# Kernel tuning notes

Measured on AMD Instinct MI355X. Metric: run time of the kernel, lower is better.

## Reference

```python
import jax, jax.numpy as jnp
import numpy as np

EPS = 1.1920928955078125e-07  # torch.finfo(float32).eps, F.rms_norm default


def rms_norm(x):
    # F.rms_norm with no learnable weight: x / sqrt(mean(x^2) + eps)
    ms = jnp.mean(jnp.square(x), axis=-1, keepdims=True)
    return x * jax.lax.rsqrt(ms + EPS)


def setup_inputs() -> dict:
    key = jax.random.key(0)
    k1, k2, k3 = jax.random.split(key, 3)
    B, L, H, S = 4, 8192, 1024, 64
    x = jax.random.normal(k1, (B, L, H), dtype=jnp.float32)
    Ws = jax.random.normal(k2, (S, H), dtype=jnp.float32) * (1.0 / np.sqrt(H))
    Wo = jax.random.normal(k3, (H, S), dtype=jnp.float32) * (1.0 / np.sqrt(S))
    return {"x": x, "Ws": Ws, "Wo": Wo}


def reference(x, Ws, Wo):
    # state_proj: (B,L,H) @ (H,S) -> (B,L,S)
    state = jnp.einsum('blh,sh->bls', x, Ws)
    # running prefix-sum over sequence dim
    state = jnp.cumsum(state, axis=1)
    # RMSNorm over last dim, then out_proj back to hidden
    return jnp.einsum('bls,hs->blh', rms_norm(state), Wo)
```

## Files before the change

### kernel.cpp

```cpp
#include <hip/hip_runtime.h>
#include <hip/hip_bf16.h>


#define BB 4
#define LL 8192
#define HH 1024
#define SS 64
#define TL 64
#define CPB (LL / TL)
#define NCHUNK (BB * CPB)
#define EPS 1.1920928955078125e-07f

typedef __attribute__((ext_vector_type(8))) short bf16x8;
typedef __attribute__((ext_vector_type(4))) float f32x4;

__device__ __forceinline__ short bf16h(float v) {
    __hip_bfloat16 b = __float2bfloat16(v);
    return __builtin_bit_cast(short, b);
}
__device__ __forceinline__ float bf16tof(short s) {
    __hip_bfloat16 b = __builtin_bit_cast(__hip_bfloat16, s);
    return __bfloat162float(b);
}

__device__ __forceinline__ void stage_load(const float* __restrict__ src, int rstride,
                                           int tid, float4* v) {
    #pragma unroll
    for (int it = 0; it < 2; ++it) {
        const int row = it * 32 + (tid >> 3);
        const int k = (tid & 7) * 8;
        const float* p = src + (long)row * rstride + k;
        v[it * 2 + 0] = *(const float4*)p;
        v[it * 2 + 1] = *(const float4*)(p + 4);
    }
}
__device__ __forceinline__ void stage_write3(const float4* v, short (*th)[72],
                                             short (*tm)[72], short (*tl)[72], int tid) {
    #pragma unroll
    for (int it = 0; it < 2; ++it) {
        const int row = it * 32 + (tid >> 3);
        const int k = (tid & 7) * 8;
        const float f[8] = {v[it*2].x, v[it*2].y, v[it*2].z, v[it*2].w,
                            v[it*2+1].x, v[it*2+1].y, v[it*2+1].z, v[it*2+1].w};
        bf16x8 h8, m8, l8;
        #pragma unroll
        for (int j = 0; j < 8; ++j) {
            const short hb = bf16h(f[j]);
            const float r1 = f[j] - bf16tof(hb);
            const short mb = bf16h(r1);
            const float r2 = r1 - bf16tof(mb);
            h8[j] = hb; m8[j] = mb; l8[j] = bf16h(r2);
        }
        *(bf16x8*)&th[row][k] = h8;
        *(bf16x8*)&tm[row][k] = m8;
        *(bf16x8*)&tl[row][k] = l8;
    }
}

#define MFMA6(ACC, AH, AM, AL, BH, BM, BL)                                        \
    ACC = __builtin_amdgcn_mfma_f32_16x16x32_bf16(AH, BH, ACC, 0, 0, 0);          \
    ACC = __builtin_amdgcn_mfma_f32_16x16x32_bf16(AH, BM, ACC, 0, 0, 0);          \
    ACC = __builtin_amdgcn_mfma_f32_16x16x32_bf16(AM, BH, ACC, 0, 0, 0);          \
    ACC = __builtin_amdgcn_mfma_f32_16x16x32_bf16(AH, BL, ACC, 0, 0, 0);          \
    ACC = __builtin_amdgcn_mfma_f32_16x16x32_bf16(AL, BH, ACC, 0, 0, 0);          \
    ACC = __builtin_amdgcn_mfma_f32_16x16x32_bf16(AM, BM, ACC, 0, 0, 0);

__global__ __launch_bounds__(256) void k_proj(const float* __restrict__ x,
                                              const float* __restrict__ Ws,
                                              float* __restrict__ state,
                                              float* __restrict__ csum)
{
    __shared__ __align__(16) short Ah[64][72], Am[64][72], Al[64][72];
    __shared__ __align__(16) short Bh[64][72], Bm[64][72], Bl[64][72];
    float (*red)[65] = (float(*)[65])Ah;

    const int tid = threadIdx.x;
    const int lane = tid & 63, w = tid >> 6;
    const int l16 = lane & 15, lg = lane >> 4;
    const int wr = w >> 1, wc = w & 1;
    const int c = blockIdx.x;
    const float* xp = x + (long)c * TL * HH;

    f32x4 acc[2][2] = {};
    float4 va[4], vb[4];
    stage_load(xp, HH, tid, va);
    stage_load(Ws, HH, tid, vb);

    for (int kt = 0; kt < HH; kt += 64) {
        stage_write3(va, Ah, Am, Al, tid);
        stage_write3(vb, Bh, Bm, Bl, tid);
        __syncthreads();
        if (kt + 64 < HH) {
            stage_load(xp + kt + 64, HH, tid, va);
            stage_load(Ws + kt + 64, HH, tid, vb);
        }
        #pragma unroll
        for (int ks = 0; ks < 2; ++ks) {
            bf16x8 ah[2], am[2], al[2], bh[2], bm[2], bl[2];
            #pragma unroll
            for (int f = 0; f < 2; ++f) {
                const int ar = wr*32 + f*16 + l16, br = wc*32 + f*16 + l16;
                const int ko = ks*32 + lg*8;
                ah[f] = *(const bf16x8*)&Ah[ar][ko];
                am[f] = *(const bf16x8*)&Am[ar][ko];
                al[f] = *(const bf16x8*)&Al[ar][ko];
                bh[f] = *(const bf16x8*)&Bh[br][ko];
                bm[f] = *(const bf16x8*)&Bm[br][ko];
                bl[f] = *(const bf16x8*)&Bl[br][ko];
            }
            #pragma unroll
            for (int fi = 0; fi < 2; ++fi)
                #pragma unroll
                for (int fj = 0; fj < 2; ++fj) {
                    MFMA6(acc[fi][fj], ah[fi], am[fi], al[fi], bh[fj], bm[fj], bl[fj])
                }
        }
        __syncthreads();
    }

    float* sp = state + (long)c * (TL * SS);
    #pragma unroll
    for (int fi = 0; fi < 2; ++fi)
        #pragma unroll
        for (int fj = 0; fj < 2; ++fj) {
            float part = 0.f;
            #pragma unroll
            for (int r = 0; r < 4; ++r) {
                const int l = wr*32 + fi*16 + lg*4 + r;
                const int s = wc*32 + fj*16 + l16;
                sp[l * SS + s] = acc[fi][fj][r];
                part += acc[fi][fj][r];
            }
            red[(wr*2 + fi)*4 + lg][wc*32 + fj*16 + l16] = part;
        }
    __syncthreads();
    if (tid < 64) {
        float t = 0.f;
        #pragma unroll
        for (int g = 0; g < 16; ++g) t += red[g][tid];
        csum[(long)c * SS + tid] = t;
    }
}

__global__ __launch_bounds__(256) void k_scan(const float* __restrict__ csum,
                                              float* __restrict__ off)
{
    const int tid = threadIdx.x;
    const int lane = tid & 63;
    const int wid = (blockIdx.x * 256 + tid) >> 6;
    const int b = wid >> 6, s = wid & 63;
    const long base = (long)b * CPB * SS + s;

    float i0 = csum[base + (long)lane * SS];
    float i1 = csum[base + (long)(lane + 64) * SS];
    #pragma unroll
    for (int d = 1; d < 64; d <<= 1) {
        float n = __shfl_up(i0, d, 64); if (lane >= d) i0 += n;
    }
    #pragma unroll
    for (int d = 1; d < 64; d <<= 1) {
        float n = __shfl_up(i1, d, 64); if (lane >= d) i1 += n;
    }
    float tot0 = __shfl(i0, 63, 64);
    float e0 = __shfl_up(i0, 1, 64); if (lane == 0) e0 = 0.f;
    float e1 = __shfl_up(i1, 1, 64); if (lane == 0) e1 = 0.f;
    e1 += tot0;
    off[base + (long)lane * SS] = e0;
    off[base + (long)(lane + 64) * SS] = e1;
}

__global__ __launch_bounds__(256) void k_out(const float* __restrict__ state,
                                             const float* __restrict__ off,
                                             const float* __restrict__ Wo,
                                             float* __restrict__ out)
{
    __shared__ __align__(16) short Ah[64][72], Am[64][72], Al[64][72];
    __shared__ __align__(16) char pool[64 * 72 * 2 * 3];
    __shared__ float ssq[4][64];
    __shared__ float scale[64];
    float (*st)[65] = (float(*)[65])pool;
    short (*Bh)[72] = (short(*)[72])pool;
    short (*Bm)[72] = (short(*)[72])(pool + 64 * 72 * 2);
    short (*Bl)[72] = (short(*)[72])(pool + 64 * 72 * 4);

    const int tid = threadIdx.x;
    const int lane = tid & 63, w = tid >> 6;
    const int l16 = lane & 15, lg = lane >> 4;
    const int wr = w >> 1, wc = w & 1;
    const int c = blockIdx.x;

    float4 vw[4];
    stage_load(Wo, SS, tid, vw);

    const float* sp = state + (long)c * (TL * SS);
    #pragma unroll
    for (int i = 0; i < 4; ++i) {
        const int e = (i * 256 + tid) * 4;
        const int l = e >> 6, s = e & 63;
        const float4 v = *(const float4*)(sp + e);
        st[l][s] = v.x; st[l][s+1] = v.y; st[l][s+2] = v.z; st[l][s+3] = v.w;
    }
    __syncthreads();

    float sq = 0.f;
    for (int i = 0; i < 16; ++i) {
        const int s = w * 16 + i;
        float v = st[lane][s];
        #pragma unroll
        for (int d = 1; d < 64; d <<= 1) {
            const float n = __shfl_up(v, d, 64);
            if (lane >= d) v += n;
        }
        v += off[(long)c * SS + s];
        st[lane][s] = v;
        sq = fmaf(v, v, sq);
    }
    ssq[w][lane] = sq;
    __syncthreads();
    if (tid < 64) {
        const float t = ssq[0][tid] + ssq[1][tid] + ssq[2][tid] + ssq[3][tid];
        scale[tid] = rsqrtf(t * (1.f / 64.f) + EPS);
    }
    __syncthreads();

    {
        const int l = tid >> 2, s0 = (tid & 3) * 16;
        const float sc = scale[l];
        #pragma unroll
        for (int blk = 0; blk < 2; ++blk) {
            bf16x8 h8, m8, l8;
            #pragma unroll
            for (int j = 0; j < 8; ++j) {
                const float v = st[l][s0 + blk*8 + j] * sc;
                const short hb = bf16h(v);
                const float r1 = v - bf16tof(hb);
                const short mb = bf16h(r1);
                const float r2 = r1 - bf16tof(mb);
                h8[j] = hb; m8[j] = mb; l8[j] = bf16h(r2);
            }
            *(bf16x8*)&Ah[l][s0 + blk*8] = h8;
            *(bf16x8*)&Am[l][s0 + blk*8] = m8;
            *(bf16x8*)&Al[l][s0 + blk*8] = l8;
        }
    }
    __syncthreads();

    bf16x8 ah[2][2], am[2][2], al[2][2];
    #pragma unroll
    for (int f = 0; f < 2; ++f)
        #pragma unroll
        for (int ks = 0; ks < 2; ++ks) {
            const int ar = wr*32 + f*16 + l16, ko = ks*32 + lg*8;
            ah[f][ks] = *(const bf16x8*)&Ah[ar][ko];
            am[f][ks] = *(const bf16x8*)&Am[ar][ko];
            al[f][ks] = *(const bf16x8*)&Al[ar][ko];
        }

    const int b = c / CPB;
    const int l0 = (c % CPB) * TL;
    float* op = out + ((long)b * LL + l0) * HH;

    for (int ht = 0; ht < HH; ht += 64) {
        stage_write3(vw, Bh, Bm, Bl, tid);
        __syncthreads();
        if (ht + 64 < HH)
            stage_load(Wo + (long)(ht + 64) * SS, SS, tid, vw);
        f32x4 acc[2][2] = {};
        #pragma unroll
        for (int ks = 0; ks < 2; ++ks) {
            bf16x8 bh[2], bm[2], bl[2];
            #pragma unroll
            for (int f = 0; f < 2; ++f) {
                const int br = wc*32 + f*16 + l16, ko = ks*32 + lg*8;
                bh[f] = *(const bf16x8*)&Bh[br][ko];
                bm[f] = *(const bf16x8*)&Bm[br][ko];
                bl[f] = *(const bf16x8*)&Bl[br][ko];
            }
            #pragma unroll
            for (int fi = 0; fi < 2; ++fi)
                #pragma unroll
                for (int fj = 0; fj < 2; ++fj) {
                    MFMA6(acc[fi][fj], ah[fi][ks], am[fi][ks], al[fi][ks],
                          bh[fj], bm[fj], bl[fj])
                }
        }
        #pragma unroll
        for (int fi = 0; fi < 2; ++fi)
            #pragma unroll
            for (int fj = 0; fj < 2; ++fj)
                #pragma unroll
                for (int r = 0; r < 4; ++r) {
                    const int l = wr*32 + fi*16 + lg*4 + r;
                    const int h = wc*32 + fj*16 + l16;
                    op[(long)l * HH + ht + h] = acc[fi][fj][r];
                }
        __syncthreads();
    }
}

extern "C" void kernel_launch(void* const* d_in, const int* in_sizes, int n_in,
                              void* d_out, int out_size, void* d_ws, size_t ws_size,
                              hipStream_t stream) {
    const float* x  = (const float*)d_in[0];
    const float* Ws = (const float*)d_in[1];
    const float* Wo = (const float*)d_in[2];
    float* out = (float*)d_out;

    float* state = (float*)d_ws;
    float* csum  = state + (size_t)NCHUNK * SS * TL;
    float* off   = csum + (size_t)NCHUNK * SS;

    k_proj<<<NCHUNK, 256, 0, stream>>>(x, Ws, state, csum);
    k_scan<<<64, 256, 0, stream>>>(csum, off);
    k_out<<<NCHUNK, 256, 0, stream>>>(state, off, Wo, out);
}
```

Measured before the change: 279.8 us.

## Pre-split weights into bf16x3 once and use 512-thread blocks

Adds a prep kernel that splits Ws and Wo into high, mid and low bf16 parts once, so the projection and output kernels load pre-split weights instead of re-splitting them in every block. Both GEMM kernels move from 4 to 8 waves per block, each wave computing a 32x16 tile rather than 32x32. This is meant to cut redundant conversion ALU work and raise latency hiding. In exchange it adds a kernel launch, extra workspace traffic for three weight copies, and more LDS reads per MFMA from the smaller per-wave tiles.

```diff
diff --git a/kernel.cpp b/kernel.cpp
--- a/kernel.cpp
+++ b/kernel.cpp
@@ -23,37 +23,14 @@
     return __bfloat162float(b);
 }
 
-__device__ __forceinline__ void stage_load(const float* __restrict__ src, int rstride,
-                                           int tid, float4* v) {
-    #pragma unroll
-    for (int it = 0; it < 2; ++it) {
-        const int row = it * 32 + (tid >> 3);
-        const int k = (tid & 7) * 8;
-        const float* p = src + (long)row * rstride + k;
-        v[it * 2 + 0] = *(const float4*)p;
-        v[it * 2 + 1] = *(const float4*)(p + 4);
-    }
-}
-__device__ __forceinline__ void stage_write3(const float4* v, short (*th)[72],
-                                             short (*tm)[72], short (*tl)[72], int tid) {
-    #pragma unroll
-    for (int it = 0; it < 2; ++it) {
-        const int row = it * 32 + (tid >> 3);
-        const int k = (tid & 7) * 8;
-        const float f[8] = {v[it*2].x, v[it*2].y, v[it*2].z, v[it*2].w,
-                            v[it*2+1].x, v[it*2+1].y, v[it*2+1].z, v[it*2+1].w};
-        bf16x8 h8, m8, l8;
-        #pragma unroll
-        for (int j = 0; j < 8; ++j) {
-            const short hb = bf16h(f[j]);
-            const float r1 = f[j] - bf16tof(hb);
-            const short mb = bf16h(r1);
-            const float r2 = r1 - bf16tof(mb);
-            h8[j] = hb; m8[j] = mb; l8[j] = bf16h(r2);
-        }
-        *(bf16x8*)&th[row][k] = h8;
-        *(bf16x8*)&tm[row][k] = m8;
-        *(bf16x8*)&tl[row][k] = l8;
+__device__ __forceinline__ void split3_8(const float* f, bf16x8& h8, bf16x8& m8, bf16x8& l8) {
+    #pragma unroll
+    for (int j = 0; j < 8; ++j) {
+        const short hb = bf16h(f[j]);
+        const float r1 = f[j] - bf16tof(hb);
+        const short mb = bf16h(r1);
+        const float r2 = r1 - bf16tof(mb);
+        h8[j] = hb; m8[j] = mb; l8[j] = bf16h(r2);
     }
 }
 
@@ -65,10 +42,33 @@
     ACC = __builtin_amdgcn_mfma_f32_16x16x32_bf16(AL, BH, ACC, 0, 0, 0);          \
     ACC = __builtin_amdgcn_mfma_f32_16x16x32_bf16(AM, BM, ACC, 0, 0, 0);
 
-__global__ __launch_bounds__(256) void k_proj(const float* __restrict__ x,
-                                              const float* __restrict__ Ws,
-                                              float* __restrict__ state,
-                                              float* __restrict__ csum)
+__global__ __launch_bounds__(512) void k_prep(const float* __restrict__ Ws,
+                                              const float* __restrict__ Wo,
+                                              short* __restrict__ wsh, short* __restrict__ wsm,
+                                              short* __restrict__ wsl, short* __restrict__ woh,
+                                              short* __restrict__ wom, short* __restrict__ wol)
+{
+    const int i = blockIdx.x * 512 + threadIdx.x;
+    {
+        const float v = Ws[i];
+        const short h = bf16h(v); const float r1 = v - bf16tof(h);
+        const short m = bf16h(r1); const float r2 = r1 - bf16tof(m);
+        wsh[i] = h; wsm[i] = m; wsl[i] = bf16h(r2);
+    }
+    {
+        const float v = Wo[i];
+        const short h = bf16h(v); const float r1 = v - bf16tof(h);
+        const short m = bf16h(r1); const float r2 = r1 - bf16tof(m);
+        woh[i] = h; wom[i] = m; wol[i] = bf16h(r2);
+    }
+}
+
+__global__ __launch_bounds__(512, 4) void k_proj(const float* __restrict__ x,
+                                                 const short* __restrict__ wsh,
+                                                 const short* __restrict__ wsm,
+                                                 const short* __restrict__ wsl,
+                                                 float* __restrict__ state,
+                                                 float* __restrict__ csum)
 {
     __shared__ __align__(16) short Ah[64][72], Am[64][72], Al[64][72];
     __shared__ __align__(16) short Bh[64][72], Bm[64][72], Bl[64][72];
@@ -77,62 +77,76 @@
     const int tid = threadIdx.x;
     const int lane = tid & 63, w = tid >> 6;
     const int l16 = lane & 15, lg = lane >> 4;
-    const int wr = w >> 1, wc = w & 1;
+    const int wr = w >> 2, wc = w & 3;
     const int c = blockIdx.x;
+    const int arow = tid >> 3, acol8 = (tid & 7) * 8;
     const float* xp = x + (long)c * TL * HH;
 
-    f32x4 acc[2][2] = {};
-    float4 va[4], vb[4];
-    stage_load(xp, HH, tid, va);
-    stage_load(Ws, HH, tid, vb);
+    f32x4 acc[2] = {};
+    float4 va[2]; bf16x8 vb[3];
+    va[0] = *(const float4*)(xp + (long)arow * HH + acol8);
+    va[1] = *(const float4*)(xp + (long)arow * HH + acol8 + 4);
+    vb[0] = *(const bf16x8*)(wsh + arow * HH + acol8);
+    vb[1] = *(const bf16x8*)(wsm + arow * HH + acol8);
+    vb[2] = *(const bf16x8*)(wsl + arow * HH + acol8);
 
     for (int kt = 0; kt < HH; kt += 64) {
-        stage_write3(va, Ah, Am, Al, tid);
-        stage_write3(vb, Bh, Bm, Bl, tid);
+        {
+            const float f8[8] = {va[0].x, va[0].y, va[0].z, va[0].w,
+                                 va[1].x, va[1].y, va[1].z, va[1].w};
+            bf16x8 h8, m8, l8;
+            split3_8(f8, h8, m8, l8);
+            *(bf16x8*)&Ah[arow][acol8] = h8;
+            *(bf16x8*)&Am[arow][acol8] = m8;
+            *(bf16x8*)&Al[arow][acol8] = l8;
+            *(bf16x8*)&Bh[arow][acol8] = vb[0];
+            *(bf16x8*)&Bm[arow][acol8] = vb[1];
+            *(bf16x8*)&Bl[arow][acol8] = vb[2];
+        }
         __syncthreads();
         if (kt + 64 < HH) {
-            stage_load(xp + kt + 64, HH, tid, va);
-            stage_load(Ws + kt + 64, HH, tid, vb);
+            va[0] = *(const float4*)(xp + (long)arow * HH + kt + 64 + acol8);
+            va[1] = *(const float4*)(xp + (long)arow * HH + kt + 64 + acol8 + 4);
+            vb[0] = *(const bf16x8*)(wsh + arow * HH + kt + 64 + acol8);
+            vb[1] = *(const bf16x8*)(wsm + arow * HH + kt + 64 + acol8);
+            vb[2] = *(const bf16x8*)(wsl + arow * HH + kt + 64 + acol8);
         }
         #pragma unroll
         for (int ks = 0; ks < 2; ++ks) {
-            bf16x8 ah[2], am[2], al[2], bh[2], bm[2], bl[2];
+            const int ko = ks * 32 + lg * 8;
+            bf16x8 ah[2], am[2], al[2];
             #pragma unroll
             for (int f = 0; f < 2; ++f) {
-                const int ar = wr*32 + f*16 + l16, br = wc*32 + f*16 + l16;
-                const int ko = ks*32 + lg*8;
+                const int ar = wr * 32 + f * 16 + l16;
                 ah[f] = *(const bf16x8*)&Ah[ar][ko];
                 am[f] = *(const bf16x8*)&Am[ar][ko];
                 al[f] = *(const bf16x8*)&Al[ar][ko];
-                bh[f] = *(const bf16x8*)&Bh[br][ko];
-                bm[f] = *(const bf16x8*)&Bm[br][ko];
-                bl[f] = *(const bf16x8*)&Bl[br][ko];
-            }
-            #pragma unroll
-            for (int fi = 0; fi < 2; ++fi)
-                #pragma unroll
-                for (int fj = 0; fj < 2; ++fj) {
-                    MFMA6(acc[fi][fj], ah[fi], am[fi], al[fi], bh[fj], bm[fj], bl[fj])
-                }
+            }
+            const int br = wc * 16 + l16;
+            const bf16x8 bh = *(const bf16x8*)&Bh[br][ko];
+            const bf16x8 bm = *(const bf16x8*)&Bm[br][ko];
+            const bf16x8 bl = *(const bf16x8*)&Bl[br][ko];
+            #pragma unroll
+            for (int fi = 0; fi < 2; ++fi) {
+                MFMA6(acc[fi], ah[fi], am[fi], al[fi], bh, bm, bl)
+            }
         }
         __syncthreads();
     }
 
     float* sp = state + (long)c * (TL * SS);
     #pragma unroll
-    for (int fi = 0; fi < 2; ++fi)
-        #pragma unroll
-        for (int fj = 0; fj < 2; ++fj) {
-            float part = 0.f;
-            #pragma unroll
-            for (int r = 0; r < 4; ++r) {
-                const int l = wr*32 + fi*16 + lg*4 + r;
-                const int s = wc*32 + fj*16 + l16;
-                sp[l * SS + s] = acc[fi][fj][r];
-                part += acc[fi][fj][r];
-            }
-            red[(wr*2 + fi)*4 + lg][wc*32 + fj*16 + l16] = part;
-        }
+    for (int fi = 0; fi < 2; ++fi) {
+        float part = 0.f;
+        #pragma unroll
+        for (int r = 0; r < 4; ++r) {
+            const int l = wr * 32 + fi * 16 + lg * 4 + r;
+            const int s = wc * 16 + l16;
+            sp[l * SS + s] = acc[fi][r];
+            part += acc[fi][r];
+        }
+        red[(wr * 2 + fi) * 4 + lg][wc * 16 + l16] = part;
+    }
     __syncthreads();
     if (tid < 64) {
         float t = 0.f;
@@ -169,14 +183,16 @@
     off[base + (long)(lane + 64) * SS] = e1;
 }
 
-__global__ __launch_bounds__(256) void k_out(const float* __restrict__ state,
-                                             const float* __restrict__ off,
-                                             const float* __restrict__ Wo,
-                                             float* __restrict__ out)
+__global__ __launch_bounds__(512, 4) void k_out(const float* __restrict__ state,
+                                                const float* __restrict__ off,
+                                                const short* __restrict__ woh,
+                                                const short* __restrict__ wom,
+                                                const short* __restrict__ wol,
+                                                float* __restrict__ out)
 {
     __shared__ __align__(16) short Ah[64][72], Am[64][72], Al[64][72];
     __shared__ __align__(16) char pool[64 * 72 * 2 * 3];
-    __shared__ float ssq[4][64];
+    __shared__ float ssq[8][64];
     __shared__ float scale[64];
     float (*st)[65] = (float(*)[65])pool;
     short (*Bh)[72] = (short(*)[72])pool;
@@ -186,16 +202,19 @@
     const int tid = threadIdx.x;
     const int lane = tid & 63, w = tid >> 6;
     const int l16 = lane & 15, lg = lane >> 4;
-    const int wr = w >> 1, wc = w & 1;
+    const int wr = w >> 2, wc = w & 3;
     const int c = blockIdx.x;
-
-    float4 vw[4];
-    stage_load(Wo, SS, tid, vw);
+    const int arow = tid >> 3, acol8 = (tid & 7) * 8;
+
+    bf16x8 vw[3];
+    vw[0] = *(const bf16x8*)(woh + arow * SS + acol8);
+    vw[1] = *(const bf16x8*)(wom + arow * SS + acol8);
+    vw[2] = *(const bf16x8*)(wol + arow * SS + acol8);
 
     const float* sp = state + (long)c * (TL * SS);
     #pragma unroll
-    for (int i = 0; i < 4; ++i) {
-        const int e = (i * 256 + tid) * 4;
+    for (int i = 0; i < 2; ++i) {
+        const int e = (i * 512 + tid) * 4;
         const int l = e >> 6, s = e & 63;
         const float4 v = *(const float4*)(sp + e);
         st[l][s] = v.x; st[l][s+1] = v.y; st[l][s+2] = v.z; st[l][s+3] = v.w;
@@ -203,8 +222,8 @@
     __syncthreads();
 
     float sq = 0.f;
-    for (int i = 0; i < 16; ++i) {
-        const int s = w * 16 + i;
+    for (int i = 0; i < 8; ++i) {
+        const int s = w * 8 + i;
         float v = st[lane][s];
         #pragma unroll
         for (int d = 1; d < 64; d <<= 1) {
@@ -218,82 +237,70 @@
     ssq[w][lane] = sq;
     __syncthreads();
     if (tid < 64) {
-        const float t = ssq[0][tid] + ssq[1][tid] + ssq[2][tid] + ssq[3][tid];
+        float t = 0.f;
+        #pragma unroll
+        for (int g = 0; g < 8; ++g) t += ssq[g][tid];
         scale[tid] = rsqrtf(t * (1.f / 64.f) + EPS);
     }
     __syncthreads();
 
     {
-        const int l = tid >> 2, s0 = (tid & 3) * 16;
+        const int l = tid >> 3, s0 = (tid & 7) * 8;
         const float sc = scale[l];
-        #pragma unroll
-        for (int blk = 0; blk < 2; ++blk) {
-            bf16x8 h8, m8, l8;
-            #pragma unroll
-            for (int j = 0; j < 8; ++j) {
-                const float v = st[l][s0 + blk*8 + j] * sc;
-                const short hb = bf16h(v);
-                const float r1 = v - bf16tof(hb);
-                const short mb = bf16h(r1);
-                const float r2 = r1 - bf16tof(mb);
-                h8[j] = hb; m8[j] = mb; l8[j] = bf16h(r2);
-            }
-            *(bf16x8*)&Ah[l][s0 + blk*8] = h8;
-            *(bf16x8*)&Am[l][s0 + blk*8] = m8;
-            *(bf16x8*)&Al[l][s0 + blk*8] = l8;
-        }
-    }
-    __syncthreads();
-
-    bf16x8 ah[2][2], am[2][2], al[2][2];
-    #pragma unroll
-    for (int f = 0; f < 2; ++f)
-        #pragma unroll
-        for (int ks = 0; ks < 2; ++ks) {
-            const int ar = wr*32 + f*16 + l16, ko = ks*32 + lg*8;
-            ah[f][ks] = *(const bf16x8*)&Ah[ar][ko];
-            am[f][ks] = *(const bf16x8*)&Am[ar][ko];
-            al[f][ks] = *(const bf16x8*)&Al[ar][ko];
-        }
+        float f8[8];
+        #pragma unroll
+        for (int j = 0; j < 8; ++j) f8[j] = st[l][s0 + j] * sc;
+        bf16x8 h8, m8, l8;
+        split3_8(f8, h8, m8, l8);
+        *(bf16x8*)&Ah[l][s0] = h8;
+        *(bf16x8*)&Am[l][s0] = m8;
+        *(bf16x8*)&Al[l][s0] = l8;
+    }
+    __syncthreads();
 
     const int b = c / CPB;
     const int l0 = (c % CPB) * TL;
     float* op = out + ((long)b * LL + l0) * HH;
 
     for (int ht = 0; ht < HH; ht += 64) {
-        stage_write3(vw, Bh, Bm, Bl, tid);
+        *(bf16x8*)&Bh[arow][acol8] = vw[0];
+        *(bf16x8*)&Bm[arow][acol8] = vw[1];
+        *(bf16x8*)&Bl[arow][acol8] = vw[2];
         __syncthreads();
-        if (ht + 64 < HH)
-            stage_load(Wo + (long)(ht + 64) * SS, SS, tid, vw);
-        f32x4 acc[2][2] = {};
+        if (ht + 64 < HH) {
+            vw[0] = *(const bf16x8*)(woh + (ht + 64 + arow) * SS + acol8);
+            vw[1] = *(const bf16x8*)(wom + (ht + 64 + arow) * SS + acol8);
+            vw[2] = *(const bf16x8*)(wol + (ht + 64 + arow) * SS + acol8);
+        }
+        f32x4 acc[2] = {};
         #pragma unroll
         for (int ks = 0; ks < 2; ++ks) {
-            bf16x8 bh[2], bm[2], bl[2];
+            const int ko = ks * 32 + lg * 8;
+            const int br = wc * 16 + l16;
+            const bf16x8 bh = *(const bf16x8*)&Bh[br][ko];
+            const bf16x8 bm = *(const bf16x8*)&Bm[br][ko];
+            const bf16x8 bl = *(const bf16x8*)&Bl[br][ko];
+            bf16x8 ah[2], am[2], al[2];
             #pragma unroll
             for (int f = 0; f < 2; ++f) {
-                const int br = wc*32 + f*16 + l16, ko = ks*32 + lg*8;
-                bh[f] = *(const bf16x8*)&Bh[br][ko];
-                bm[f] = *(const bf16x8*)&Bm[br][ko];
-                bl[f] = *(const bf16x8*)&Bl[br][ko];
-            }
-            #pragma unroll
-            for (int fi = 0; fi < 2; ++fi)
-                #pragma unroll
-                for (int fj = 0; fj < 2; ++fj) {
-                    MFMA6(acc[fi][fj], ah[fi][ks], am[fi][ks], al[fi][ks],
-                          bh[fj], bm[fj], bl[fj])
-                }
+                const int ar = wr * 32 + f * 16 + l16;
+                ah[f] = *(const bf16x8*)&Ah[ar][ko];
+                am[f] = *(const bf16x8*)&Am[ar][ko];
+                al[f] = *(const bf16x8*)&Al[ar][ko];
+            }
+            #pragma unroll
+            for (int fi = 0; fi < 2; ++fi) {
+                MFMA6(acc[fi], ah[fi], am[fi], al[fi], bh, bm, bl)
+            }
         }
         #pragma unroll
         for (int fi = 0; fi < 2; ++fi)
             #pragma unroll
-            for (int fj = 0; fj < 2; ++fj)
-                #pragma unroll
-                for (int r = 0; r < 4; ++r) {
-                    const int l = wr*32 + fi*16 + lg*4 + r;
-                    const int h = wc*32 + fj*16 + l16;
-                    op[(long)l * HH + ht + h] = acc[fi][fj][r];
-                }
+            for (int r = 0; r < 4; ++r) {
+                const int l = wr * 32 + fi * 16 + lg * 4 + r;
+                const int h = wc * 16 + l16;
+                op[(long)l * HH + ht + h] = acc[fi][r];
+            }
         __syncthreads();
     }
 }
@@ -309,8 +316,15 @@
     float* state = (float*)d_ws;
     float* csum  = state + (size_t)NCHUNK * SS * TL;
     float* off   = csum + (size_t)NCHUNK * SS;
-
-    k_proj<<<NCHUNK, 256, 0, stream>>>(x, Ws, state, csum);
+    short* wsh = (short*)(off + (size_t)NCHUNK * SS);
+    short* wsm = wsh + (size_t)SS * HH;
+    short* wsl = wsm + (size_t)SS * HH;
+    short* woh = wsl + (size_t)SS * HH;
+    short* wom = woh + (size_t)HH * SS;
+    short* wol = wom + (size_t)HH * SS;
+
+    k_prep<<<128, 512, 0, stream>>>(Ws, Wo, wsh, wsm, wsl, woh, wom, wol);
+    k_proj<<<NCHUNK, 512, 0, stream>>>(x, wsh, wsm, wsl, state, csum);
     k_scan<<<64, 256, 0, stream>>>(csum, off);
-    k_out<<<NCHUNK, 256, 0, stream>>>(state, off, Wo, out);
-}
+    k_out<<<NCHUNK, 512, 0, stream>>>(state, off, woh, wom, wol, out);
+}
```

After: 276.7 us. About the same (-1.1%).
